# Performance work log

Hardware: AMD Instinct MI355X
Metric: run time of the kernel (lower is better)

## Reference

```python
import jax, jax.numpy as jnp
import numpy as np

B, T, C = 2, 2048, 1024
NUM_HEADS, NUM_KV_HEADS, HEAD_DIM = 16, 8, 64
R = NUM_HEADS // NUM_KV_HEADS  # q heads per kv head
WINDOW = 512
HIDDEN = 4096
SOFT_CAP = 50.0


def setup_inputs() -> dict:
    key = jax.random.key(0)
    ks = jax.random.split(key, 10)
    std = 0.02
    return {
        "x": jax.random.normal(ks[0], (B, T, C), jnp.float32),
        "kurtosis_sum": jnp.zeros((), jnp.float32),
        "rms1_scale": jnp.zeros((C,), jnp.float32),
        "q_kernel": std * jax.random.normal(ks[1], (C, R, NUM_KV_HEADS, HEAD_DIM), jnp.float32),
        "k_kernel": std * jax.random.normal(ks[2], (C, NUM_KV_HEADS, HEAD_DIM), jnp.float32),
        "v_kernel": std * jax.random.normal(ks[3], (C, NUM_KV_HEADS, HEAD_DIM), jnp.float32),
        "out_kernel": std * jax.random.normal(ks[4], (R, NUM_KV_HEADS, HEAD_DIM, C), jnp.float32),
        "rms2_scale": jnp.zeros((C,), jnp.float32),
        "gate_kernel": std * jax.random.normal(ks[5], (C, HIDDEN), jnp.float32),
        "up_kernel": std * jax.random.normal(ks[6], (C, HIDDEN), jnp.float32),
        "down_kernel": std * jax.random.normal(ks[7], (HIDDEN, C), jnp.float32),
    }


def sine_table(features, length, max_timescale=1e6):
    fraction = jnp.arange(0, features, 2, dtype=jnp.float32) / features
    rot_freq = 1.0 / (max_timescale ** fraction)
    sinusoid = jnp.arange(length, dtype=jnp.float32)[:, None] * rot_freq[None, :]
    sinusoid = jnp.concatenate([sinusoid, sinusoid], axis=-1)  # (T, features)
    return jnp.sin(sinusoid), jnp.cos(sinusoid)


def rotate_half(x):
    x1, x2 = jnp.split(x, 2, axis=-1)
    return jnp.concatenate([-x2, x1], axis=-1)


def rms_norm(x, scale):
    var = jnp.mean(jnp.square(x.astype(jnp.float32)), axis=-1, keepdims=True)
    normed = (x * jax.lax.rsqrt(var + 1e-6)).astype(x.dtype)
    return normed * (1 + scale)


def excess_kurtosis(emb):
    mean = jnp.mean(emb, axis=-1, keepdims=True)
    std = jnp.std(emb, axis=-1, keepdims=True)
    centralized = emb - mean
    fourth = jnp.mean(centralized ** 4, axis=-1, keepdims=True)
    kurt = jnp.squeeze(fourth / (std ** 4 + 1e-6), axis=-1).reshape(-1) - 3
    return jnp.sum(jnp.maximum(kurt, 0.0))


def reference(x, kurtosis_sum, rms1_scale, q_kernel, k_kernel, v_kernel,
              out_kernel, rms2_scale, gate_kernel, up_kernel, down_kernel):
    Bc, Tc, Cc = x.shape
    # sliding-window causal mask: j <= i and |i - j| < WINDOW
    idx = jnp.arange(Tc)
    causal = idx[:, None] >= idx[None, :]
    band = jnp.abs(idx[:, None] - idx[None, :]) < WINDOW
    mask = (causal & band)[None, None, None]  # (1,1,1,T,T) for brhsd scores

    # --- attention ---
    attn_in = rms_norm(x, rms1_scale)
    q = jnp.einsum('bsm,mrhk->brhsk', attn_in, q_kernel)
    k = jnp.einsum('bdm,mhk->bhdk', attn_in, k_kernel)
    v = jnp.einsum('bdm,mhv->bhdv', attn_in, v_kernel)

    sin, cos = sine_table(HEAD_DIM, Tc, max_timescale=1e6)
    q = q * cos[None, None, None] + rotate_half(q) * sin[None, None, None]
    k = k * cos[None, None] + rotate_half(k) * sin[None, None]

    scale = jax.lax.rsqrt(jnp.asarray(HEAD_DIM, dtype=x.dtype))
    qk = jnp.einsum('brhsk,bhdk->brhsd', q, k) * scale
    qk = jnp.tanh(qk / SOFT_CAP) * SOFT_CAP
    probs = jax.nn.softmax(qk.astype(jnp.float32), where=mask).astype(x.dtype)
    qkv = jnp.einsum('brhsd,bhdv->brhsv', probs, v)
    attn_out = jnp.einsum('brhsv,rhvm->bsm', qkv, out_kernel)
    x = x + attn_out

    # --- SwiGLU MLP ---
    mlp_in = rms_norm(x, rms2_scale)
    gate = jax.nn.silu(mlp_in @ gate_kernel)
    up = mlp_in @ up_kernel
    x = x + (up * gate) @ down_kernel

    return (x, kurtosis_sum + excess_kurtosis(x))
```

## Files before the change

kernel.cpp:

```cpp
#include <hip/hip_runtime.h>
#include <hip/hip_bf16.h>

typedef __attribute__((ext_vector_type(8))) short short8;
typedef __attribute__((ext_vector_type(4))) float f32x4;
typedef __attribute__((ext_vector_type(4))) int int4v;
typedef __attribute__((ext_vector_type(8))) int int8v;

#define DEVFN static __device__ __forceinline__

DEVFN float bf2f(unsigned short u) {
    unsigned int i = ((unsigned int)u) << 16;
    float f; __builtin_memcpy(&f, &i, 4); return f;
}
DEVFN unsigned short f2bf(float f) {
    unsigned int i; __builtin_memcpy(&i, &f, 4);
    unsigned int r = i + 0x7fffu + ((i >> 16) & 1u);
    return (unsigned short)(r >> 16);
}
DEVFN unsigned char f2fp8(float f) {
    int r = __builtin_amdgcn_cvt_pk_fp8_f32(f, f, 0, false);
    return (unsigned char)(r & 0xff);
}
DEVFN float fastrcp(float x) { return __builtin_amdgcn_rcpf(x); }

DEVFN void load_lds16(const void* g, void* l) {
    __builtin_amdgcn_global_load_lds(
        (__attribute__((address_space(1))) void*)g,
        (__attribute__((address_space(3))) void*)l, 16, 0, 0);
}

DEVFN f32x4 mfma_fp8(int8v a, int8v b, f32x4 c) {
    return __builtin_amdgcn_mfma_scale_f32_16x16x128_f8f6f4(
        a, b, c, 0, 0, 0, 0x7F7F7F7F, 0, 0x7F7F7F7F);
}

constexpr int Bsz = 2, T = 2048, C = 1024;
constexpr int NH = 16, NKV = 8, HD = 64;
constexpr int HID = 4096;
constexpr int NTOK = Bsz * T;
constexpr size_t MiB = 1024 * 1024;

constexpr size_t OFF_WQKV = 0;
constexpr size_t OFF_WOUT = 4 * MiB;
constexpr size_t OFF_WGATE = 6 * MiB;
constexpr size_t OFF_WUP = 10 * MiB;
constexpr size_t OFF_WDOWN = 14 * MiB;
constexpr size_t OFF_XN1 = 18 * MiB;
constexpr size_t OFF_QKVP = 26 * MiB;
constexpr size_t OFF_P2 = 26 * MiB;
constexpr size_t OFF_QB = 58 * MiB;
constexpr size_t OFF_KB = 66 * MiB;
constexpr size_t OFF_VT = 70 * MiB;
constexpr size_t OFF_CTX = 74 * MiB;
constexpr size_t OFF_X2 = 82 * MiB;
constexpr size_t OFF_XN2 = 98 * MiB;
constexpr size_t OFF_G = 102 * MiB;
constexpr size_t OFF_P4 = 118 * MiB;

__global__ __launch_bounds__(256) void prep_kernel(
    const float* __restrict__ qk, const float* __restrict__ kk2,
    const float* __restrict__ vk, const float* __restrict__ ok,
    const float* __restrict__ gk, const float* __restrict__ uk,
    const float* __restrict__ dk,
    unsigned short* __restrict__ wqkv, unsigned short* __restrict__ wout,
    unsigned char* __restrict__ wgate, unsigned char* __restrict__ wup,
    unsigned char* __restrict__ wdown,
    const float* __restrict__ x, const float* __restrict__ rms1_scale,
    unsigned short* __restrict__ xn1) {
    __shared__ float t[32][33];
    __shared__ float red[4];
    int id = blockIdx.x;
    int tid = threadIdx.x;
    if (id >= 15360) {
        int row = id - 15360;
        const float4 v = *(const float4*)&x[(size_t)row * 1024 + tid * 4];
        float ss = v.x * v.x + v.y * v.y + v.z * v.z + v.w * v.w;
#pragma unroll
        for (int m = 32; m; m >>= 1) ss += __shfl_xor(ss, m, 64);
        if ((tid & 63) == 0) red[tid >> 6] = ss;
        __syncthreads();
        float tot = red[0] + red[1] + red[2] + red[3];
        float inv = rsqrtf(tot * (1.f / 1024.f) + 1e-6f);
        const float4 sc = *(const float4*)&rms1_scale[tid * 4];
        size_t o = (size_t)row * 1024 + tid * 4;
        xn1[o + 0] = f2bf(v.x * inv * (1.f + sc.x));
        xn1[o + 1] = f2bf(v.y * inv * (1.f + sc.y));
        xn1[o + 2] = f2bf(v.z * inv * (1.f + sc.z));
        xn1[o + 3] = f2bf(v.w * inv * (1.f + sc.w));
        return;
    }
    const float* in; int K, N, nx, base; int fp8 = 0;
    unsigned short* out16 = nullptr; unsigned char* out8 = nullptr;
    if (id < 1024)       { in = qk;  out16 = wqkv;                       K = 1024; N = 1024; nx = 32;  base = 0; }
    else if (id < 1536)  { in = kk2; out16 = wqkv + (size_t)1024 * 1024; K = 1024; N = 512;  nx = 16;  base = 1024; }
    else if (id < 2048)  { in = vk;  out16 = wqkv + (size_t)1536 * 1024; K = 1024; N = 512;  nx = 16;  base = 1536; }
    else if (id < 3072)  { in = ok;  out16 = wout;                       K = 1024; N = 1024; nx = 32;  base = 2048; }
    else if (id < 7168)  { in = gk;  out8 = wgate; fp8 = 1;              K = 1024; N = 4096; nx = 128; base = 3072; }
    else if (id < 11264) { in = uk;  out8 = wup; fp8 = 1;                K = 1024; N = 4096; nx = 128; base = 7168; }
    else                 { in = dk;  out8 = wdown; fp8 = 1;              K = 4096; N = 1024; nx = 32;  base = 11264; }
    int lid = id - base;
    int n0 = (lid % nx) * 32, k0 = (lid / nx) * 32;
    int tx = tid & 31, ty = tid >> 5;
#pragma unroll
    for (int i = 0; i < 4; i++)
        t[ty + 8 * i][tx] = in[(size_t)(k0 + ty + 8 * i) * N + n0 + tx];
    __syncthreads();
    if (fp8) {
#pragma unroll
        for (int i = 0; i < 4; i++)
            out8[(size_t)(n0 + ty + 8 * i) * K + k0 + tx] = f2fp8(t[tx][ty + 8 * i] * 16.f);
    } else {
#pragma unroll
        for (int i = 0; i < 4; i++)
            out16[(size_t)(n0 + ty + 8 * i) * K + k0 + tx] = f2bf(t[tx][ty + 8 * i]);
    }
}

__global__ __launch_bounds__(256) void gemm128(const unsigned short* __restrict__ A,
                                               const unsigned short* __restrict__ Bt,
                                               unsigned short* __restrict__ Cp,
                                               int N, int K, int lda, int ldb,
                                               size_t zA, size_t zB, size_t zC) {
    __shared__ __align__(16) unsigned short As[128 * 32];
    __shared__ __align__(16) unsigned short Bs[128 * 32];
    A += (size_t)blockIdx.z * zA;
    Bt += (size_t)blockIdx.z * zB;
    const int tid = threadIdx.x;
    const int lane = tid & 63, w = tid >> 6;
    const int quad = lane >> 4, l15 = lane & 15;
    const int wr = w >> 1, wc = w & 1;
    const int m0 = blockIdx.y * 128, n0 = blockIdx.x * 128;

    f32x4 acc[4][4];
#pragma unroll
    for (int i = 0; i < 4; i++)
#pragma unroll
        for (int j = 0; j < 4; j++) acc[i][j] = f32x4{0.f, 0.f, 0.f, 0.f};

    const int stRow = (w << 4) + (lane >> 2);
    const int stCol = (lane & 3) << 3;

    for (int kk = 0; kk < K; kk += 32) {
#pragma unroll
        for (int i = 0; i < 2; i++) {
            load_lds16(A + (size_t)(m0 + (i << 6) + stRow) * lda + kk + stCol,
                       &As[((i << 6) + (w << 4)) * 32]);
            load_lds16(Bt + (size_t)(n0 + (i << 6) + stRow) * ldb + kk + stCol,
                       &Bs[((i << 6) + (w << 4)) * 32]);
        }
        __syncthreads();
        short8 a[4], b[4];
#pragma unroll
        for (int mi = 0; mi < 4; mi++)
            a[mi] = *(const short8*)&As[(wr * 64 + mi * 16 + l15) * 32 + quad * 8];
#pragma unroll
        for (int ni = 0; ni < 4; ni++)
            b[ni] = *(const short8*)&Bs[(wc * 64 + ni * 16 + l15) * 32 + quad * 8];
#pragma unroll
        for (int mi = 0; mi < 4; mi++)
#pragma unroll
            for (int ni = 0; ni < 4; ni++)
                acc[mi][ni] = __builtin_amdgcn_mfma_f32_16x16x32_bf16(a[mi], b[ni], acc[mi][ni], 0, 0, 0);
        __syncthreads();
    }
#pragma unroll
    for (int mi = 0; mi < 4; mi++)
#pragma unroll
        for (int ni = 0; ni < 4; ni++)
#pragma unroll
            for (int r = 0; r < 4; r++) {
                int row = m0 + wr * 64 + mi * 16 + quad * 4 + r;
                int col = n0 + wc * 64 + ni * 16 + l15;
                Cp[(size_t)blockIdx.z * zC + (size_t)row * N + col] = f2bf(acc[mi][ni][r]);
            }
}

DEVFN int8v read_frag8(const unsigned char* buf, int rb, int quad) {
    int base = rb * 128;
    int h0 = (2 * quad) ^ (rb & 7);
    int h1 = (2 * quad + 1) ^ (rb & 7);
    int4v lo = *(const int4v*)&buf[base + h0 * 16];
    int4v hi = *(const int4v*)&buf[base + h1 * 16];
    return int8v{lo.x, lo.y, lo.z, lo.w, hi.x, hi.y, hi.z, hi.w};
}

__global__ __launch_bounds__(256) void gateup_kernel(const unsigned char* __restrict__ A,
                                                     const unsigned char* __restrict__ Bg,
                                                     const unsigned char* __restrict__ Bu,
                                                     unsigned char* __restrict__ out) {
    __shared__ __align__(16) unsigned char As[128 * 128];
    __shared__ __align__(16) unsigned char Gs[64 * 128];
    __shared__ __align__(16) unsigned char Us[64 * 128];
    const int tid = threadIdx.x;
    const int lane = tid & 63, w = tid >> 6;
    const int quad = lane >> 4, l15 = lane & 15;
    const int wr = w >> 1, wc = w & 1;
    const int m0 = blockIdx.y * 128, n0 = blockIdx.x * 64;

    f32x4 aG[4][2], aU[4][2];
#pragma unroll
    for (int i = 0; i < 4; i++)
#pragma unroll
        for (int j = 0; j < 2; j++) { aG[i][j] = f32x4{0.f, 0.f, 0.f, 0.f}; aU[i][j] = f32x4{0.f, 0.f, 0.f, 0.f}; }

    const int lrow = lane >> 3;
    const int hA = (lane & 7) ^ lrow;

    for (int kk = 0; kk < 1024; kk += 128) {
#pragma unroll
        for (int j = 0; j < 4; j++) {
            int i = w * 4 + j;
            int r = i * 8 + lrow;
            load_lds16(A + (size_t)(m0 + r) * 1024 + kk + hA * 16, &As[i * 1024]);
        }
#pragma unroll
        for (int j = 0; j < 2; j++) {
            int i = w * 2 + j;
            int r = i * 8 + lrow;
            load_lds16(Bg + (size_t)(n0 + r) * 1024 + kk + hA * 16, &Gs[i * 1024]);
            load_lds16(Bu + (size_t)(n0 + r) * 1024 + kk + hA * 16, &Us[i * 1024]);
        }
        __syncthreads();
        int8v a[4], bg[2], bu[2];
#pragma unroll
        for (int mi = 0; mi < 4; mi++)
            a[mi] = read_frag8(As, wr * 64 + mi * 16 + l15, quad);
#pragma unroll
        for (int ni = 0; ni < 2; ni++) {
            bg[ni] = read_frag8(Gs, wc * 32 + ni * 16 + l15, quad);
            bu[ni] = read_frag8(Us, wc * 32 + ni * 16 + l15, quad);
        }
#pragma unroll
        for (int mi = 0; mi < 4; mi++)
#pragma unroll
            for (int ni = 0; ni < 2; ni++) {
                aG[mi][ni] = mfma_fp8(a[mi], bg[ni], aG[mi][ni]);
                aU[mi][ni] = mfma_fp8(a[mi], bu[ni], aU[mi][ni]);
            }
        __syncthreads();
    }
#pragma unroll
    for (int mi = 0; mi < 4; mi++)
#pragma unroll
        for (int ni = 0; ni < 2; ni++)
#pragma unroll
            for (int r = 0; r < 4; r++) {
                int row = m0 + wr * 64 + mi * 16 + quad * 4 + r;
                int col = n0 + wc * 32 + ni * 16 + l15;
                float vg = aG[mi][ni][r] * (1.f / 64.f);
                float vu = aU[mi][ni][r] * (1.f / 64.f);
                float s = vg * fastrcp(1.f + __expf(-vg));
                out[(size_t)row * 4096 + col] = f2fp8(s * vu * 8.f);
            }
}

__global__ __launch_bounds__(256) void down_gemm(const unsigned char* __restrict__ A,
                                                 const unsigned char* __restrict__ Bt,
                                                 unsigned short* __restrict__ Cp) {
    __shared__ __align__(16) unsigned char As[128 * 128];
    __shared__ __align__(16) unsigned char Bs[128 * 128];
    const int tid = threadIdx.x;
    const int lane = tid & 63, w = tid >> 6;
    const int quad = lane >> 4, l15 = lane & 15;
    const int wr = w >> 1, wc = w & 1;
    const int m0 = blockIdx.y * 128, n0 = blockIdx.x * 128;
    const int kbase = blockIdx.z * 1024;

    f32x4 acc[4][4];
#pragma unroll
    for (int i = 0; i < 4; i++)
#pragma unroll
        for (int j = 0; j < 4; j++) acc[i][j] = f32x4{0.f, 0.f, 0.f, 0.f};

    const int lrow = lane >> 3;
    const int hA = (lane & 7) ^ lrow;

    for (int kk = 0; kk < 1024; kk += 128) {
#pragma unroll
        for (int j = 0; j < 4; j++) {
            int i = w * 4 + j;
            int r = i * 8 + lrow;
            load_lds16(A + (size_t)(m0 + r) * 4096 + kbase + kk + hA * 16, &As[i * 1024]);
            load_lds16(Bt + (size_t)(n0 + r) * 4096 + kbase + kk + hA * 16, &Bs[i * 1024]);
        }
        __syncthreads();
        int8v a[4], b[4];
#pragma unroll
        for (int mi = 0; mi < 4; mi++)
            a[mi] = read_frag8(As, wr * 64 + mi * 16 + l15, quad);
#pragma unroll
        for (int ni = 0; ni < 4; ni++)
            b[ni] = read_frag8(Bs, wc * 64 + ni * 16 + l15, quad);
#pragma unroll
        for (int mi = 0; mi < 4; mi++)
#pragma unroll
            for (int ni = 0; ni < 4; ni++)
                acc[mi][ni] = mfma_fp8(a[mi], b[ni], acc[mi][ni]);
        __syncthreads();
    }
    const size_t Z = (size_t)NTOK * 1024;
#pragma unroll
    for (int mi = 0; mi < 4; mi++)
#pragma unroll
        for (int ni = 0; ni < 4; ni++)
#pragma unroll
            for (int r = 0; r < 4; r++) {
                int row = m0 + wr * 64 + mi * 16 + quad * 4 + r;
                int col = n0 + wc * 64 + ni * 16 + l15;
                Cp[(size_t)blockIdx.z * Z + (size_t)row * 1024 + col] =
                    f2bf(acc[mi][ni][r] * (1.f / 128.f));
            }
}

__global__ __launch_bounds__(256) void reduce_out(const unsigned short* __restrict__ p,
                                                  const float* __restrict__ x,
                                                  const float* __restrict__ scale,
                                                  float* __restrict__ x2,
                                                  unsigned char* __restrict__ xn2,
                                                  const float* __restrict__ ksum,
                                                  float* __restrict__ outk) {
    __shared__ float red[4];
    int row = blockIdx.x, tid = threadIdx.x;
    if (row == 0 && tid == 0) outk[0] = ksum[0];
    size_t base = (size_t)row * 1024 + tid * 4;
    const size_t Z = (size_t)NTOK * 1024;
    float4 v = *(const float4*)&x[base];
#pragma unroll
    for (int z = 0; z < 4; z++) {
        ushort4 u = *(const ushort4*)&p[base + z * Z];
        v.x += bf2f(u.x); v.y += bf2f(u.y); v.z += bf2f(u.z); v.w += bf2f(u.w);
    }
    *(float4*)&x2[base] = v;
    float ss = v.x * v.x + v.y * v.y + v.z * v.z + v.w * v.w;
#pragma unroll
    for (int m = 32; m; m >>= 1) ss += __shfl_xor(ss, m, 64);
    if ((tid & 63) == 0) red[tid >> 6] = ss;
    __syncthreads();
    float tot = red[0] + red[1] + red[2] + red[3];
    float inv = rsqrtf(tot * (1.f / 1024.f) + 1e-6f) * 4.f;
    const float4 sc = *(const float4*)&scale[tid * 4];
    xn2[base + 0] = f2fp8(v.x * inv * (1.f + sc.x));
    xn2[base + 1] = f2fp8(v.y * inv * (1.f + sc.y));
    xn2[base + 2] = f2fp8(v.z * inv * (1.f + sc.z));
    xn2[base + 3] = f2fp8(v.w * inv * (1.f + sc.w));
}

__global__ __launch_bounds__(256) void reduce_down(const unsigned short* __restrict__ p,
                                                   const float* __restrict__ x2,
                                                   float* __restrict__ outx,
                                                   float* __restrict__ outk) {
    __shared__ float red[4], r2[4], r4[4];
    int row = blockIdx.x, tid = threadIdx.x;
    size_t base = (size_t)row * 1024 + tid * 4;
    const size_t Z = (size_t)NTOK * 1024;
    float4 v = *(const float4*)&x2[base];
#pragma unroll
    for (int z = 0; z < 4; z++) {
        ushort4 u = *(const ushort4*)&p[base + z * Z];
        v.x += bf2f(u.x); v.y += bf2f(u.y); v.z += bf2f(u.z); v.w += bf2f(u.w);
    }
    *(float4*)&outx[base] = v;
    float s = v.x + v.y + v.z + v.w;
#pragma unroll
    for (int m = 32; m; m >>= 1) s += __shfl_xor(s, m, 64);
    if ((tid & 63) == 0) red[tid >> 6] = s;
    __syncthreads();
    float mean = (red[0] + red[1] + red[2] + red[3]) * (1.f / 1024.f);
    float cx = v.x - mean, cy = v.y - mean, cz = v.z - mean, cw = v.w - mean;
    float x2v = cx * cx, y2 = cy * cy, z2 = cz * cz, w2 = cw * cw;
    float c2 = x2v + y2 + z2 + w2;
    float c4 = x2v * x2v + y2 * y2 + z2 * z2 + w2 * w2;
#pragma unroll
    for (int m = 32; m; m >>= 1) {
        c2 += __shfl_xor(c2, m, 64);
        c4 += __shfl_xor(c4, m, 64);
    }
    if ((tid & 63) == 0) { r2[tid >> 6] = c2; r4[tid >> 6] = c4; }
    __syncthreads();
    if (tid == 0) {
        float m2 = (r2[0] + r2[1] + r2[2] + r2[3]) * (1.f / 1024.f);
        float m4 = (r4[0] + r4[1] + r4[2] + r4[3]) * (1.f / 1024.f);
        float kurt = m4 / (m2 * m2 + 1e-6f) - 3.f;
        if (kurt > 0.f) atomicAdd(outk, kurt);
    }
}

__global__ __launch_bounds__(256) void ropevt_kernel(const unsigned short* __restrict__ qkvp,
                                                     unsigned short* __restrict__ qb,
                                                     unsigned short* __restrict__ kb,
                                                     unsigned short* __restrict__ vt) {
    __shared__ float sv[32], cv[32];
    __shared__ unsigned short tile[64][68];
    const size_t Z = (size_t)NTOK * 2048;
    int id = blockIdx.x;
    int tid = threadIdx.x;
    if (id < NTOK) {
        int tok = id;
        int b = tok >> 11, t = tok & 2047;
        if (tid < 32) {
            float fr = (float)tid * (1.f / 32.f);
            float freq = powf(1e6f, -fr);
            float a = (float)t * freq;
            sv[tid] = sinf(a);
            cv[tid] = cosf(a);
        }
        __syncthreads();
        const unsigned short* r0 = qkvp + (size_t)tok * 2048;
        const unsigned short* r1 = r0 + Z;
#pragma unroll
        for (int e = tid; e < 1536; e += 256) {
            int u = e >> 6, d = e & 63;
            int col = (u < 16) ? (u * 64 + d) : (1024 + (u - 16) * 64 + d);
            int pcol = (d < 32) ? col + 32 : col - 32;
            float sgn = (d < 32) ? -1.f : 1.f;
            float vc = bf2f(r0[col]) + bf2f(r1[col]);
            float vp = bf2f(r0[pcol]) + bf2f(r1[pcol]);
            float o = vc * cv[d & 31] + sgn * vp * sv[d & 31];
            if (u < 16)
                qb[((size_t)(b * 16 + u) * 2048 + t) * 64 + d] = f2bf(o);
            else
                kb[((size_t)(b * 8 + (u - 16)) * 2048 + t) * 64 + d] = f2bf(o);
        }
    } else {
        int lid = id - NTOK;
        int b = lid >> 8, h = (lid >> 5) & 7, t0 = (lid & 31) * 64;
        int d = tid & 63, tr = tid >> 6;
#pragma unroll
        for (int i = 0; i < 16; i++) {
            int t = tr + i * 4;
            size_t gi = (size_t)(b * 2048 + t0 + t) * 2048 + 1536 + h * 64 + d;
            tile[t][d] = f2bf(bf2f(qkvp[gi]) + bf2f(qkvp[gi + Z]));
        }
        __syncthreads();
        int tt = tid & 63, dr = tid >> 6;
#pragma unroll
        for (int i = 0; i < 16; i++) {
            int dd = dr + i * 4;
            vt[((size_t)(b * 8 + h) * 64 + dd) * 2048 + t0 + tt] = tile[tt][dd];
        }
    }
}

__global__ __launch_bounds__(256) void attn_kernel(const unsigned short* __restrict__ qb,
                                                   const unsigned short* __restrict__ kb,
                                                   const unsigned short* __restrict__ vt,
                                                   unsigned short* __restrict__ ctx) {
    __shared__ __align__(16) unsigned short Ks[64 * 64];
    __shared__ __align__(16) unsigned short Vs[64 * 64];
    __shared__ __align__(16) unsigned short P[4][2][16 * 64];
    const int tid = threadIdx.x, lane = tid & 63, w = tid >> 6;
    const int quad = lane >> 4, l15 = lane & 15;
    const int qt = blockIdx.x, H = blockIdx.y, b = blockIdx.z;
    const int hkv = H & 7;
    const int qw = qt * 64 + w * 16;

    const unsigned short* qbase = qb + ((size_t)(b * 16 + H) * 2048 + qw) * 64;
    short8 aq0 = *(const short8*)(qbase + (size_t)l15 * 64 + quad * 8);
    short8 aq1 = *(const short8*)(qbase + (size_t)l15 * 64 + 32 + quad * 8);

    const unsigned short* kbase = kb + (size_t)(b * 8 + hkv) * 2048 * 64;
    const unsigned short* vbase = vt + (size_t)(b * 8 + hkv) * 64 * 2048;

    const short bf1 = (short)0x3F80;
    const short8 ones = {bf1, bf1, bf1, bf1, bf1, bf1, bf1, bf1};

    f32x4 O[4];
#pragma unroll
    for (int i = 0; i < 4; i++) O[i] = f32x4{0.f, 0.f, 0.f, 0.f};
    f32x4 lacc = f32x4{0.f, 0.f, 0.f, 0.f};

    const int srow = lane >> 3;
    const int schunk = (lane & 7) ^ srow;
    const int sw = l15 & 7;

    int kstartB = qt * 64 - 511;
    if (kstartB < 0) kstartB = 0;
    kstartB &= ~63;
    const int kendB = qt * 64 + 63;
    int buf = 0;

    for (int k0 = kstartB; k0 <= kendB; k0 += 64) {
#pragma unroll
        for (int rr = 0; rr < 2; rr++) {
            int row = w * 8 + rr * 32 + srow;
            load_lds16(kbase + (size_t)(k0 + row) * 64 + schunk * 8,
                       &Ks[(w * 8 + rr * 32) * 64]);
            load_lds16(vbase + (size_t)row * 2048 + k0 + schunk * 8,
                       &Vs[(w * 8 + rr * 32) * 64]);
        }
        __syncthreads();
        f32x4 S[4];
#pragma unroll
        for (int c = 0; c < 4; c++) {
            const unsigned short* kp = &Ks[(c * 16 + l15) * 64];
            short8 kf0 = *(const short8*)&kp[(quad ^ sw) * 8];
            short8 kf1 = *(const short8*)&kp[((4 + quad) ^ sw) * 8];
            f32x4 s = __builtin_amdgcn_mfma_f32_16x16x32_bf16(aq0, kf0, f32x4{0.f, 0.f, 0.f, 0.f}, 0, 0, 0);
            s = __builtin_amdgcn_mfma_f32_16x16x32_bf16(aq1, kf1, s, 0, 0, 0);
            S[c] = s;
        }
        unsigned short* Pw = P[w][buf];
#pragma unroll
        for (int c = 0; c < 4; c++)
#pragma unroll
            for (int r = 0; r < 4; r++) {
                int i = qw + quad * 4 + r;
                int j = k0 + c * 16 + l15;
                float Sc = fminf(3200.f, fmaxf(-3200.f, S[c][r]));
                float e = __expf(Sc * 0.005f);
                float y = 50.f - 100.f * fastrcp(e + 1.f);
                bool ok = (j <= i) && ((i - j) < 512);
                float pv = ok ? __expf(y) : 0.f;
                Pw[(quad * 4 + r) * 64 + c * 16 + l15] = f2bf(pv);
            }
        asm volatile("s_waitcnt lgkmcnt(0)" ::: "memory");
        short8 pf0 = *(const short8*)&Pw[l15 * 64 + quad * 8];
        short8 pf1 = *(const short8*)&Pw[l15 * 64 + 32 + quad * 8];
#pragma unroll
        for (int ni = 0; ni < 4; ni++) {
            const unsigned short* vp = &Vs[(ni * 16 + l15) * 64];
            short8 vf0 = *(const short8*)&vp[(quad ^ sw) * 8];
            short8 vf1 = *(const short8*)&vp[((4 + quad) ^ sw) * 8];
            O[ni] = __builtin_amdgcn_mfma_f32_16x16x32_bf16(pf0, vf0, O[ni], 0, 0, 0);
            O[ni] = __builtin_amdgcn_mfma_f32_16x16x32_bf16(pf1, vf1, O[ni], 0, 0, 0);
        }
        lacc = __builtin_amdgcn_mfma_f32_16x16x32_bf16(pf0, ones, lacc, 0, 0, 0);
        lacc = __builtin_amdgcn_mfma_f32_16x16x32_bf16(pf1, ones, lacc, 0, 0, 0);
        buf ^= 1;
        __syncthreads();
    }
#pragma unroll
    for (int r = 0; r < 4; r++) {
        float inv = fastrcp(lacc[r]);
        int i = qw + quad * 4 + r;
        size_t tok = (size_t)b * 2048 + i;
#pragma unroll
        for (int ni = 0; ni < 4; ni++)
            ctx[tok * 1024 + H * 64 + ni * 16 + l15] = f2bf(O[ni][r] * inv);
    }
}

extern "C" void kernel_launch(void* const* d_in, const int* in_sizes, int n_in,
                              void* d_out, int out_size, void* d_ws, size_t ws_size,
                              hipStream_t stream) {
    const float* x = (const float*)d_in[0];
    const float* ksum = (const float*)d_in[1];
    const float* rms1_scale = (const float*)d_in[2];
    const float* q_w = (const float*)d_in[3];
    const float* k_w = (const float*)d_in[4];
    const float* v_w = (const float*)d_in[5];
    const float* out_w = (const float*)d_in[6];
    const float* rms2_scale = (const float*)d_in[7];
    const float* gate_w = (const float*)d_in[8];
    const float* up_w = (const float*)d_in[9];
    const float* down_w = (const float*)d_in[10];

    char* ws = (char*)d_ws;
    unsigned short* wqkv = (unsigned short*)(ws + OFF_WQKV);
    unsigned short* wout = (unsigned short*)(ws + OFF_WOUT);
    unsigned char* wgate = (unsigned char*)(ws + OFF_WGATE);
    unsigned char* wup = (unsigned char*)(ws + OFF_WUP);
    unsigned char* wdown = (unsigned char*)(ws + OFF_WDOWN);
    unsigned short* xn1 = (unsigned short*)(ws + OFF_XN1);
    unsigned short* qkvp = (unsigned short*)(ws + OFF_QKVP);
    unsigned short* p2 = (unsigned short*)(ws + OFF_P2);
    unsigned short* qb = (unsigned short*)(ws + OFF_QB);
    unsigned short* kb = (unsigned short*)(ws + OFF_KB);
    unsigned short* vtb = (unsigned short*)(ws + OFF_VT);
    unsigned short* ctx = (unsigned short*)(ws + OFF_CTX);
    float* x2 = (float*)(ws + OFF_X2);
    unsigned char* xn2 = (unsigned char*)(ws + OFF_XN2);
    unsigned char* g = (unsigned char*)(ws + OFF_G);
    unsigned short* p4 = (unsigned short*)(ws + OFF_P4);
    float* outx = (float*)d_out;
    float* outk = outx + (size_t)NTOK * C;

    prep_kernel<<<15360 + NTOK, 256, 0, stream>>>(
        q_w, k_w, v_w, out_w, gate_w, up_w, down_w,
        wqkv, wout, wgate, wup, wdown, x, rms1_scale, xn1);

    gemm128<<<dim3(2048 / 128, NTOK / 128, 2), 256, 0, stream>>>(
        xn1, wqkv, qkvp, 2048, 512, 1024, 1024, 512, 512, (size_t)NTOK * 2048);

    ropevt_kernel<<<NTOK + 512, 256, 0, stream>>>(qkvp, qb, kb, vtb);

    attn_kernel<<<dim3(T / 64, NH, Bsz), 256, 0, stream>>>(qb, kb, vtb, ctx);

    gemm128<<<dim3(1024 / 128, NTOK / 128, 4), 256, 0, stream>>>(
        ctx, wout, p2, 1024, 256, 1024, 1024, 256, 256, (size_t)NTOK * 1024);
    reduce_out<<<NTOK, 256, 0, stream>>>(p2, x, rms2_scale, x2, xn2, ksum, outk);

    gateup_kernel<<<dim3(HID / 64, NTOK / 128), 256, 0, stream>>>(xn2, wgate, wup, g);

    down_gemm<<<dim3(1024 / 128, NTOK / 128, 4), 256, 0, stream>>>(g, wdown, p4);
    reduce_down<<<NTOK, 256, 0, stream>>>(p4, x2, outx, outk);

    (void)in_sizes; (void)n_in; (void)out_size; (void)ws_size;
}
```

Baseline: 345.2 us.

## Double-buffer LDS tiles in gate/up and down FP8 GEMMs with async prefetch

Both FP8 MLP GEMM kernels now keep two LDS buffers and prefetch the K-tile two steps ahead with direct-to-LDS loads. Manual vmcnt/lgkmcnt waits and barriers replace the two __syncthreads per iteration, and the loop is fully unrolled. The MFMA block is raised in wave priority so global loads overlap compute. This doubles LDS use per block (64KB), which can lower occupancy. The vmcnt(8) count assumes a fixed number of loads per stage.

```diff
diff --git a/kernel.cpp b/kernel.cpp
--- a/kernel.cpp
+++ b/kernel.cpp
@@ -188,9 +188,9 @@
                                                      const unsigned char* __restrict__ Bg,
                                                      const unsigned char* __restrict__ Bu,
                                                      unsigned char* __restrict__ out) {
-    __shared__ __align__(16) unsigned char As[128 * 128];
-    __shared__ __align__(16) unsigned char Gs[64 * 128];
-    __shared__ __align__(16) unsigned char Us[64 * 128];
+    __shared__ __align__(16) unsigned char As[2][128 * 128];
+    __shared__ __align__(16) unsigned char Gs[2][64 * 128];
+    __shared__ __align__(16) unsigned char Us[2][64 * 128];
     const int tid = threadIdx.x;
     const int lane = tid & 63, w = tid >> 6;
     const int quad = lane >> 4, l15 = lane & 15;
@@ -206,30 +206,43 @@
     const int lrow = lane >> 3;
     const int hA = (lane & 7) ^ lrow;
 
-    for (int kk = 0; kk < 1024; kk += 128) {
+    auto STAGE = [&](int t, int b) {
 #pragma unroll
         for (int j = 0; j < 4; j++) {
             int i = w * 4 + j;
             int r = i * 8 + lrow;
-            load_lds16(A + (size_t)(m0 + r) * 1024 + kk + hA * 16, &As[i * 1024]);
+            load_lds16(A + (size_t)(m0 + r) * 1024 + t * 128 + hA * 16, &As[b][i * 1024]);
         }
 #pragma unroll
         for (int j = 0; j < 2; j++) {
             int i = w * 2 + j;
             int r = i * 8 + lrow;
-            load_lds16(Bg + (size_t)(n0 + r) * 1024 + kk + hA * 16, &Gs[i * 1024]);
-            load_lds16(Bu + (size_t)(n0 + r) * 1024 + kk + hA * 16, &Us[i * 1024]);
-        }
-        __syncthreads();
+            load_lds16(Bg + (size_t)(n0 + r) * 1024 + t * 128 + hA * 16, &Gs[b][i * 1024]);
+            load_lds16(Bu + (size_t)(n0 + r) * 1024 + t * 128 + hA * 16, &Us[b][i * 1024]);
+        }
+    };
+
+    STAGE(0, 0);
+    STAGE(1, 1);
+
+#pragma unroll
+    for (int t = 0; t < 8; ++t) {
+        if (t < 7) asm volatile("s_waitcnt vmcnt(8)\n\ts_barrier" ::: "memory");
+        else       asm volatile("s_waitcnt vmcnt(0)\n\ts_barrier" ::: "memory");
+        const int b = t & 1;
         int8v a[4], bg[2], bu[2];
 #pragma unroll
         for (int mi = 0; mi < 4; mi++)
-            a[mi] = read_frag8(As, wr * 64 + mi * 16 + l15, quad);
+            a[mi] = read_frag8(As[b], wr * 64 + mi * 16 + l15, quad);
 #pragma unroll
         for (int ni = 0; ni < 2; ni++) {
-            bg[ni] = read_frag8(Gs, wc * 32 + ni * 16 + l15, quad);
-            bu[ni] = read_frag8(Us, wc * 32 + ni * 16 + l15, quad);
-        }
+            bg[ni] = read_frag8(Gs[b], wc * 32 + ni * 16 + l15, quad);
+            bu[ni] = read_frag8(Us[b], wc * 32 + ni * 16 + l15, quad);
+        }
+        asm volatile("s_waitcnt lgkmcnt(0)\n\ts_barrier" ::: "memory");
+        if (t < 6) STAGE(t + 2, b);
+        __builtin_amdgcn_sched_barrier(0);
+        __builtin_amdgcn_s_setprio(1);
 #pragma unroll
         for (int mi = 0; mi < 4; mi++)
 #pragma unroll
@@ -237,7 +250,7 @@
                 aG[mi][ni] = mfma_fp8(a[mi], bg[ni], aG[mi][ni]);
                 aU[mi][ni] = mfma_fp8(a[mi], bu[ni], aU[mi][ni]);
             }
-        __syncthreads();
+        __builtin_amdgcn_s_setprio(0);
     }
 #pragma unroll
     for (int mi = 0; mi < 4; mi++)
@@ -257,8 +270,8 @@
 __global__ __launch_bounds__(256) void down_gemm(const unsigned char* __restrict__ A,
                                                  const unsigned char* __restrict__ Bt,
                                                  unsigned short* __restrict__ Cp) {
-    __shared__ __align__(16) unsigned char As[128 * 128];
-    __shared__ __align__(16) unsigned char Bs[128 * 128];
+    __shared__ __align__(16) unsigned char As[2][128 * 128];
+    __shared__ __align__(16) unsigned char Bs[2][128 * 128];
     const int tid = threadIdx.x;
     const int lane = tid & 63, w = tid >> 6;
     const int quad = lane >> 4, l15 = lane & 15;
@@ -275,28 +288,41 @@
     const int lrow = lane >> 3;
     const int hA = (lane & 7) ^ lrow;
 
-    for (int kk = 0; kk < 1024; kk += 128) {
+    auto STAGE = [&](int t, int b) {
 #pragma unroll
         for (int j = 0; j < 4; j++) {
             int i = w * 4 + j;
             int r = i * 8 + lrow;
-            load_lds16(A + (size_t)(m0 + r) * 4096 + kbase + kk + hA * 16, &As[i * 1024]);
-            load_lds16(Bt + (size_t)(n0 + r) * 4096 + kbase + kk + hA * 16, &Bs[i * 1024]);
-        }
-        __syncthreads();
-        int8v a[4], b[4];
+            load_lds16(A + (size_t)(m0 + r) * 4096 + kbase + t * 128 + hA * 16, &As[b][i * 1024]);
+            load_lds16(Bt + (size_t)(n0 + r) * 4096 + kbase + t * 128 + hA * 16, &Bs[b][i * 1024]);
+        }
+    };
+
+    STAGE(0, 0);
+    STAGE(1, 1);
+
+#pragma unroll
+    for (int t = 0; t < 8; ++t) {
+        if (t < 7) asm volatile("s_waitcnt vmcnt(8)\n\ts_barrier" ::: "memory");
+        else       asm volatile("s_waitcnt vmcnt(0)\n\ts_barrier" ::: "memory");
+        const int b = t & 1;
+        int8v a[4], bb[4];
 #pragma unroll
         for (int mi = 0; mi < 4; mi++)
-            a[mi] = read_frag8(As, wr * 64 + mi * 16 + l15, quad);
+            a[mi] = read_frag8(As[b], wr * 64 + mi * 16 + l15, quad);
 #pragma unroll
         for (int ni = 0; ni < 4; ni++)
-            b[ni] = read_frag8(Bs, wc * 64 + ni * 16 + l15, quad);
+            bb[ni] = read_frag8(Bs[b], wc * 64 + ni * 16 + l15, quad);
+        asm volatile("s_waitcnt lgkmcnt(0)\n\ts_barrier" ::: "memory");
+        if (t < 6) STAGE(t + 2, b);
+        __builtin_amdgcn_sched_barrier(0);
+        __builtin_amdgcn_s_setprio(1);
 #pragma unroll
         for (int mi = 0; mi < 4; mi++)
 #pragma unroll
             for (int ni = 0; ni < 4; ni++)
-                acc[mi][ni] = mfma_fp8(a[mi], b[ni], acc[mi][ni]);
-        __syncthreads();
+                acc[mi][ni] = mfma_fp8(a[mi], bb[ni], acc[mi][ni]);
+        __builtin_amdgcn_s_setprio(0);
     }
     const size_t Z = (size_t)NTOK * 1024;
 #pragma unroll
```

New measurement: 339.2 us. About the same (-1.7%).
